# Kernel optimization log

Measured on AMD Instinct MI355X. Metric: run time of the kernel, lower is better.

The kernel has to match this reference:

```python
import jax, jax.numpy as jnp
import numpy as np

B, C, H, W, N = 16, 80, 100, 100, 32
LAMBDA_L1, LAMBDA_GIOU, POS_IOU_THR = 1.0, 2.0, 0.3
# pos_radius=1.5 with python int() truncation on non-negative max_i/max_j gives
# window rows/cols in [idx-2, idx+1] clipped to the grid (verified vs torch code).
R_LO, R_HI = 2, 1


def _make_boxes(key, shape):
    kc, ks = jax.random.split(key)
    c = jax.random.uniform(kc, shape + (2,), minval=0.1, maxval=0.9)
    s = jax.random.uniform(ks, shape + (2,), minval=0.05, maxval=0.3)
    return jnp.concatenate([c - s * 0.5, c + s * 0.5], axis=-1)  # valid xyxy


def setup_inputs() -> dict:
    key = jax.random.key(0)
    k1, k2, k3 = jax.random.split(key, 3)
    pred_boxes = _make_boxes(k1, (B, C, H, W))        # [B,C,H,W,4]
    gt_boxes = _make_boxes(k2, (B, N))                # [B,N,4]
    gt_labels = jax.random.randint(k3, (B, N), 0, C)  # [B,N] in [0,C)
    return {"pred_boxes": pred_boxes, "gt_boxes": gt_boxes, "gt_labels": gt_labels}


def giou_fn(a, b):
    # a: [...,4], b broadcastable [...,4], xyxy. Same math as torchvision generalized_box_iou.
    area_a = (a[..., 2] - a[..., 0]) * (a[..., 3] - a[..., 1])
    area_b = (b[..., 2] - b[..., 0]) * (b[..., 3] - b[..., 1])
    lt = jnp.maximum(a[..., :2], b[..., :2])
    rb = jnp.minimum(a[..., 2:], b[..., 2:])
    wh = jnp.clip(rb - lt, 0.0)
    inter = wh[..., 0] * wh[..., 1]
    union = area_a + area_b - inter
    iou = inter / union
    lt_c = jnp.minimum(a[..., :2], b[..., :2])
    rb_c = jnp.maximum(a[..., 2:], b[..., 2:])
    wh_c = jnp.clip(rb_c - lt_c, 0.0)
    area_c = wh_c[..., 0] * wh_c[..., 1]
    return iou - (area_c - union) / area_c


def reference(pred_boxes, gt_boxes, gt_labels):
    _, _, h, w, _ = pred_boxes.shape
    rows = jnp.arange(h)
    cols = jnp.arange(w)

    def per_gt(pred_img, gt_box, label):
        # pred_img: [C,H,W,4], gt_box: [4], label: scalar int
        grid = pred_img[label]                      # [H,W,4] gather over class dim
        g = giou_fn(grid, gt_box)                   # [H,W] GIoU vs this GT
        flat = g.reshape(-1)
        idx = jnp.argmax(flat)                      # row-major, matches torch argmax on [H,W]
        max_iou = flat[idx]
        mi, mj = idx // w, idx % w
        rmask = (rows >= mi - R_LO) & (rows <= jnp.minimum(mi + R_HI, h - 1))
        cmask = (cols >= mj - R_LO) & (cols <= jnp.minimum(mj + R_HI, w - 1))
        mask = (rmask[:, None] & cmask[None, :]).astype(grid.dtype)  # [H,W] window
        valid = (max_iou > POS_IOU_THR).astype(grid.dtype)
        l1 = jnp.abs(grid - gt_box).mean(-1)        # F.l1_loss per cell (mean over 4 coords)
        return (valid * jnp.sum(l1 * mask),
                valid * jnp.sum((1.0 - g) * mask),
                valid * jnp.sum(mask))

    per_img = jax.vmap(per_gt, in_axes=(None, 0, 0))   # over N GTs
    l1s, gious, cnts = jax.vmap(per_img)(pred_boxes, gt_boxes, gt_labels)  # over B
    n_pos = jnp.sum(cnts)
    denom = jnp.maximum(n_pos, 1.0)
    loss_l1 = jnp.sum(l1s) / denom
    loss_giou = jnp.sum(gious) / denom
    loss_total = LAMBDA_L1 * loss_l1 + LAMBDA_GIOU * loss_giou
    return loss_total
```

## Files before the change

### kernel.cpp

```cpp
#include <hip/hip_runtime.h>

constexpr int B_ = 16, C_ = 80, H_ = 100, W_ = 100, N_ = 32;
constexpr int HW = H_ * W_;
constexpr int BN = B_ * N_;
constexpr float POS_THR = 0.3f;
constexpr int TPB = 1024;

__device__ __forceinline__ float rcpf(float x) { return __builtin_amdgcn_rcpf(x); }

__device__ __forceinline__ float giou4(const float4 a,
                                       const float gx0, const float gy0,
                                       const float gx1, const float gy1,
                                       const float area_b) {
    float area_a = (a.z - a.x) * (a.w - a.y);
    float ltx = fmaxf(a.x, gx0), lty = fmaxf(a.y, gy0);
    float rbx = fminf(a.z, gx1), rby = fminf(a.w, gy1);
    float iw = fmaxf(rbx - ltx, 0.0f), ih = fmaxf(rby - lty, 0.0f);
    float inter = iw * ih;
    float uni = area_a + area_b - inter;
    float cx0 = fminf(a.x, gx0), cy0 = fminf(a.y, gy0);
    float cx1 = fmaxf(a.z, gx1), cy1 = fmaxf(a.w, gy1);
    float area_c = (cx1 - cx0) * (cy1 - cy0);
    return inter * rcpf(uni) + uni * rcpf(area_c) - 1.0f;
}

__global__ __launch_bounds__(TPB) void per_gt_kernel(
    const float* __restrict__ pred,
    const float* __restrict__ gt,
    const int*   __restrict__ labels,
    float* __restrict__ ws)
{
    const int bn = blockIdx.x;
    const int b  = bn / N_;
    const int label = labels[bn];
    const float4 g4 = reinterpret_cast<const float4*>(gt)[bn];
    const float area_b = (g4.z - g4.x) * (g4.w - g4.y);
    const float4* __restrict__ base =
        reinterpret_cast<const float4*>(pred) + ((size_t)b * C_ + label) * HW;

    float best = -3.0f;
    int   bi   = HW;
    for (int i = threadIdx.x; i < HW; i += TPB) {
        float g = giou4(base[i], g4.x, g4.y, g4.z, g4.w, area_b);
        if (g > best) { best = g; bi = i; }
    }

    #pragma unroll
    for (int off = 32; off; off >>= 1) {
        float ov = __shfl_down(best, off, 64);
        int   oi = __shfl_down(bi,   off, 64);
        if (ov > best || (ov == best && oi < bi)) { best = ov; bi = oi; }
    }

    __shared__ float sv[16];
    __shared__ int   si[16];
    const int wid  = threadIdx.x >> 6;
    const int lane = threadIdx.x & 63;
    if (lane == 0) { sv[wid] = best; si[wid] = bi; }
    __syncthreads();

    if (wid == 0) {
        best = (lane < 16) ? sv[lane] : -3.0f;
        bi   = (lane < 16) ? si[lane] : HW;
        #pragma unroll
        for (int off = 8; off; off >>= 1) {
            float ov = __shfl_down(best, off, 16);
            int   oi = __shfl_down(bi,   off, 16);
            if (ov > best || (ov == best && oi < bi)) { best = ov; bi = oi; }
        }
        best = __shfl(best, 0, 64);
        bi   = __shfl(bi,   0, 64);

        float sl1 = 0.0f, sg = 0.0f, ct = 0.0f;
        if (best > POS_THR) {
            const int mi = bi / W_, mj = bi % W_;
            const int r0 = max(mi - 2, 0), r1 = min(mi + 1, H_ - 1);
            const int c0 = max(mj - 2, 0), c1 = min(mj + 1, W_ - 1);
            const int r = r0 + (lane >> 2);
            const int c = c0 + (lane & 3);
            if (lane < 16 && r <= r1 && c <= c1) {
                float4 a = base[r * W_ + c];
                float g = giou4(a, g4.x, g4.y, g4.z, g4.w, area_b);
                sl1 = 0.25f * (fabsf(a.x - g4.x) + fabsf(a.y - g4.y) +
                               fabsf(a.z - g4.z) + fabsf(a.w - g4.w));
                sg = 1.0f - g;
                ct = 1.0f;
            }
            #pragma unroll
            for (int off = 8; off; off >>= 1) {
                sl1 += __shfl_down(sl1, off, 16);
                sg  += __shfl_down(sg,  off, 16);
                ct  += __shfl_down(ct,  off, 16);
            }
        }
        if (lane == 0) {
            ws[bn]          = sl1;
            ws[BN + bn]     = sg;
            ws[2 * BN + bn] = ct;
        }
    }
}

__global__ __launch_bounds__(BN) void finalize_kernel(
    const float* __restrict__ ws, float* __restrict__ out)
{
    const int t = threadIdx.x;
    float l1 = ws[t], gi = ws[BN + t], ct = ws[2 * BN + t];
    #pragma unroll
    for (int off = 32; off; off >>= 1) {
        l1 += __shfl_down(l1, off, 64);
        gi += __shfl_down(gi, off, 64);
        ct += __shfl_down(ct, off, 64);
    }
    __shared__ float s0[8], s1[8], s2[8];
    const int wid = t >> 6;
    if ((t & 63) == 0) { s0[wid] = l1; s1[wid] = gi; s2[wid] = ct; }
    __syncthreads();
    if (t == 0) {
        float L = 0.0f, G = 0.0f, Cn = 0.0f;
        #pragma unroll
        for (int w = 0; w < BN / 64; ++w) { L += s0[w]; G += s1[w]; Cn += s2[w]; }
        const float denom = fmaxf(Cn, 1.0f);
        out[0] = L / denom + 2.0f * (G / denom);
    }
}

extern "C" void kernel_launch(void* const* d_in, const int* in_sizes, int n_in,
                              void* d_out, int out_size, void* d_ws, size_t ws_size,
                              hipStream_t stream) {
    const float* pred   = (const float*)d_in[0];
    const float* gt     = (const float*)d_in[1];
    const int*   labels = (const int*)d_in[2];
    float* ws  = (float*)d_ws;
    float* out = (float*)d_out;

    per_gt_kernel<<<BN, TPB, 0, stream>>>(pred, gt, labels, ws);
    finalize_kernel<<<1, BN, 0, stream>>>(ws, out);
}
```

Baseline: 21.65 us.

## Fuse finalize into per-GT kernel via last-block atomic counter and unroll scan

Drops the separate finalize kernel launch. Each block publishes its partial sums, increments an atomic counter, and the last block to finish does the global reduction and writes the loss. A memset of the counter is added to the stream. The argmax scan is also unrolled by two so each thread has two float4 loads in flight. The cost is an extra memset operation plus threadfence and atomic traffic.

```diff
diff --git a/kernel.cpp b/kernel.cpp
--- a/kernel.cpp
+++ b/kernel.cpp
@@ -28,7 +28,8 @@
     const float* __restrict__ pred,
     const float* __restrict__ gt,
     const int*   __restrict__ labels,
-    float* __restrict__ ws)
+    float* __restrict__ ws,
+    float* __restrict__ out)
 {
     const int bn = blockIdx.x;
     const int b  = bn / N_;
@@ -40,7 +41,16 @@
 
     float best = -3.0f;
     int   bi   = HW;
-    for (int i = threadIdx.x; i < HW; i += TPB) {
+    int i = threadIdx.x;
+    for (; i + TPB < HW; i += 2 * TPB) {
+        float4 a0 = base[i];
+        float4 a1 = base[i + TPB];
+        float g0 = giou4(a0, g4.x, g4.y, g4.z, g4.w, area_b);
+        float g1 = giou4(a1, g4.x, g4.y, g4.z, g4.w, area_b);
+        if (g0 > best) { best = g0; bi = i; }
+        if (g1 > best) { best = g1; bi = i + TPB; }
+    }
+    if (i < HW) {
         float g = giou4(base[i], g4.x, g4.y, g4.z, g4.w, area_b);
         if (g > best) { best = g; bi = i; }
     }
@@ -59,69 +69,71 @@
     if (lane == 0) { sv[wid] = best; si[wid] = bi; }
     __syncthreads();
 
-    if (wid == 0) {
-        best = (lane < 16) ? sv[lane] : -3.0f;
-        bi   = (lane < 16) ? si[lane] : HW;
+    if (wid != 0) return;
+
+    best = (lane < 16) ? sv[lane] : -3.0f;
+    bi   = (lane < 16) ? si[lane] : HW;
+    #pragma unroll
+    for (int off = 8; off; off >>= 1) {
+        float ov = __shfl_down(best, off, 16);
+        int   oi = __shfl_down(bi,   off, 16);
+        if (ov > best || (ov == best && oi < bi)) { best = ov; bi = oi; }
+    }
+    best = __shfl(best, 0, 64);
+    bi   = __shfl(bi,   0, 64);
+
+    float sl1 = 0.0f, sg = 0.0f, ct = 0.0f;
+    if (best > POS_THR) {
+        const int mi = bi / W_, mj = bi % W_;
+        const int r0 = max(mi - 2, 0), r1 = min(mi + 1, H_ - 1);
+        const int c0 = max(mj - 2, 0), c1 = min(mj + 1, W_ - 1);
+        const int r = r0 + (lane >> 2);
+        const int c = c0 + (lane & 3);
+        if (lane < 16 && r <= r1 && c <= c1) {
+            float4 a = base[r * W_ + c];
+            float g = giou4(a, g4.x, g4.y, g4.z, g4.w, area_b);
+            sl1 = 0.25f * (fabsf(a.x - g4.x) + fabsf(a.y - g4.y) +
+                           fabsf(a.z - g4.z) + fabsf(a.w - g4.w));
+            sg = 1.0f - g;
+            ct = 1.0f;
+        }
         #pragma unroll
         for (int off = 8; off; off >>= 1) {
-            float ov = __shfl_down(best, off, 16);
-            int   oi = __shfl_down(bi,   off, 16);
-            if (ov > best || (ov == best && oi < bi)) { best = ov; bi = oi; }
-        }
-        best = __shfl(best, 0, 64);
-        bi   = __shfl(bi,   0, 64);
-
-        float sl1 = 0.0f, sg = 0.0f, ct = 0.0f;
-        if (best > POS_THR) {
-            const int mi = bi / W_, mj = bi % W_;
-            const int r0 = max(mi - 2, 0), r1 = min(mi + 1, H_ - 1);
-            const int c0 = max(mj - 2, 0), c1 = min(mj + 1, W_ - 1);
-            const int r = r0 + (lane >> 2);
-            const int c = c0 + (lane & 3);
-            if (lane < 16 && r <= r1 && c <= c1) {
-                float4 a = base[r * W_ + c];
-                float g = giou4(a, g4.x, g4.y, g4.z, g4.w, area_b);
-                sl1 = 0.25f * (fabsf(a.x - g4.x) + fabsf(a.y - g4.y) +
-                               fabsf(a.z - g4.z) + fabsf(a.w - g4.w));
-                sg = 1.0f - g;
-                ct = 1.0f;
-            }
-            #pragma unroll
-            for (int off = 8; off; off >>= 1) {
-                sl1 += __shfl_down(sl1, off, 16);
-                sg  += __shfl_down(sg,  off, 16);
-                ct  += __shfl_down(ct,  off, 16);
-            }
-        }
-        if (lane == 0) {
-            ws[bn]          = sl1;
-            ws[BN + bn]     = sg;
-            ws[2 * BN + bn] = ct;
+            sl1 += __shfl_down(sl1, off, 16);
+            sg  += __shfl_down(sg,  off, 16);
+            ct  += __shfl_down(ct,  off, 16);
         }
     }
-}
 
-__global__ __launch_bounds__(BN) void finalize_kernel(
-    const float* __restrict__ ws, float* __restrict__ out)
-{
-    const int t = threadIdx.x;
-    float l1 = ws[t], gi = ws[BN + t], ct = ws[2 * BN + t];
+    unsigned old = 0;
+    if (lane == 0) {
+        ws[bn]          = sl1;
+        ws[BN + bn]     = sg;
+        ws[2 * BN + bn] = ct;
+        __threadfence();
+        old = atomicAdd((unsigned*)(ws + 3 * BN), 1u);
+    }
+    old = __shfl(old, 0, 64);
+    if (old != BN - 1) return;
+
+    __threadfence();
+    float l1 = 0.0f, gi = 0.0f, cn = 0.0f;
+    #pragma unroll
+    for (int k = 0; k < BN / 64; ++k) {
+        const int idx = lane + k * 64;
+        l1 += ws[idx];
+        gi += ws[BN + idx];
+        cn += ws[2 * BN + idx];
+    }
     #pragma unroll
     for (int off = 32; off; off >>= 1) {
         l1 += __shfl_down(l1, off, 64);
         gi += __shfl_down(gi, off, 64);
-        ct += __shfl_down(ct, off, 64);
+        cn += __shfl_down(cn, off, 64);
     }
-    __shared__ float s0[8], s1[8], s2[8];
-    const int wid = t >> 6;
-    if ((t & 63) == 0) { s0[wid] = l1; s1[wid] = gi; s2[wid] = ct; }
-    __syncthreads();
-    if (t == 0) {
-        float L = 0.0f, G = 0.0f, Cn = 0.0f;
-        #pragma unroll
-        for (int w = 0; w < BN / 64; ++w) { L += s0[w]; G += s1[w]; Cn += s2[w]; }
-        const float denom = fmaxf(Cn, 1.0f);
-        out[0] = L / denom + 2.0f * (G / denom);
+    if (lane == 0) {
+        const float denom = fmaxf(cn, 1.0f);
+        out[0] = l1 / denom + 2.0f * (gi / denom);
     }
 }
 
@@ -134,6 +146,6 @@
     float* ws  = (float*)d_ws;
     float* out = (float*)d_out;
 
-    per_gt_kernel<<<BN, TPB, 0, stream>>>(pred, gt, labels, ws);
-    finalize_kernel<<<1, BN, 0, stream>>>(ws, out);
+    hipMemsetAsync(ws + 3 * BN, 0, sizeof(unsigned), stream);
+    per_gt_kernel<<<BN, TPB, 0, stream>>>(pred, gt, labels, ws, out);
 }
```

After: 33.70 us. 55.7% more time.
